# Performance work log

Hardware: AMD Instinct MI355X
Metric: run time of the kernel (lower is better)

## Reference

```python
import jax, jax.numpy as jnp
import numpy as np

B, S, V = 2048, 200, 50257
E, H, EMB = 60, 30, 20  # encode_size, hidden_size, embed_size


def setup_inputs() -> dict:
    key = jax.random.key(0)
    ks = jax.random.split(key, 24)
    emb = jax.random.normal(ks[7], (V, EMB), jnp.float32) * 0.02
    emb = emb.at[3].set(0.0)  # padding_idx=3
    inp = {
        'coverage': jax.random.uniform(ks[0], (B, S), jnp.float32),
        'enc_out': jax.random.normal(ks[1], (B, S, E), jnp.float32),
        'h0': jax.random.normal(ks[2], (1, B, H), jnp.float32),
        'c0': jax.random.normal(ks[3], (1, B, H), jnp.float32),
        'attn': jax.random.uniform(ks[4], (B, S), jnp.float32),
        'dec_input': jax.random.randint(ks[5], (B, 1), 0, V, jnp.int32),
        'enc_inputs': jax.random.randint(ks[6], (B, S), 0, V, jnp.int32),
        'embedding': emb,
        # LSTM (torch gate order i,f,g,o)
        'w_ih': jax.random.normal(ks[8], (4 * H, EMB + E), jnp.float32) * 0.1,
        'w_hh': jax.random.normal(ks[9], (4 * H, H), jnp.float32) * 0.1,
        'b_ih': jax.random.normal(ks[10], (4 * H,), jnp.float32) * 0.1,
        'b_hh': jax.random.normal(ks[11], (4 * H,), jnp.float32) * 0.1,
        # Attention submodule
        'attn_wh_w': jax.random.normal(ks[12], (H, E), jnp.float32) * 0.1,
        'attn_wh_b': jax.random.normal(ks[13], (H,), jnp.float32) * 0.1,
        'attn_ws_w': jax.random.normal(ks[14], (H, H), jnp.float32) * 0.1,
        'attn_ws_b': jax.random.normal(ks[15], (H,), jnp.float32) * 0.1,
        'attn_wc': jax.random.uniform(ks[16], (H,), jnp.float32),
        'attn_v': jax.random.uniform(ks[17], (H,), jnp.float32),
        # pointer-gen params
        'wh': jax.random.uniform(ks[18], (E,), jnp.float32),
        'ws': jax.random.uniform(ks[19], (H,), jnp.float32),
        'wx': jax.random.uniform(ks[20], (EMB,), jnp.float32),
        'v_w': jax.random.normal(ks[21], (V, H), jnp.float32) * 0.02,
        'v_b': jax.random.normal(ks[22], (V,), jnp.float32) * 0.02,
    }
    return inp


def reference(coverage, enc_out, h0, c0, attn, dec_input, enc_inputs, embedding,
              w_ih, w_hh, b_ih, b_hh, attn_wh_w, attn_wh_b, attn_ws_w, attn_ws_b,
              attn_wc, attn_v, wh, ws, wx, v_w, v_b):
    # context = bmm(attn[B,1,S], enc_out[B,S,E]) -> [B,E]
    context = jnp.einsum('bs,bse->be', attn, enc_out)
    embed = embedding[dec_input[:, 0]]              # [B,EMB]
    x = jnp.concatenate([context, embed], axis=-1)  # [B,E+EMB]
    # single-step LSTM (torch gate order i,f,g,o)
    gates = x @ w_ih.T + b_ih + h0[0] @ w_hh.T + b_hh
    i, f, g, o = jnp.split(gates, 4, axis=-1)
    c = jax.nn.sigmoid(f) * c0[0] + jax.nn.sigmoid(i) * jnp.tanh(g)
    h = jax.nn.sigmoid(o) * jnp.tanh(c)             # rnn_out [B,H]
    p_vocab = jax.nn.softmax(h @ v_w.T + v_b, axis=1)   # [B,V]
    p_gen = jax.nn.sigmoid(context @ wh + h @ ws + embed @ wx)[:, None]  # [B,1]
    # attention
    wh_app = enc_out @ attn_wh_w.T + attn_wh_b      # [B,S,H]
    ws_app = (h @ attn_ws_w.T + attn_ws_b)[:, None, :]  # [B,1,H]
    wc_app = coverage[..., None] * attn_wc          # [B,S,H]
    energy = jnp.tanh(wh_app + ws_app + wc_app) @ attn_v  # [B,S]
    new_attn = jax.nn.softmax(energy, axis=1)
    coverage_loss = jnp.sum(jnp.minimum(new_attn, coverage))
    new_coverage = coverage + new_attn
    # scatter copy-attention into vocab space (duplicate idx: arbitrary winner, as torch scatter_)
    rows = jnp.arange(enc_inputs.shape[0])[:, None]
    attn_scores = jnp.zeros((enc_inputs.shape[0], v_w.shape[0]), p_vocab.dtype).at[rows, enc_inputs].set(new_attn)
    output = p_gen * p_vocab + (1.0 - p_gen) * attn_scores
    return output, new_coverage, (h[None], c[None]), new_attn, coverage_loss
```

## Files before the change

### kernel.cpp

```cpp
#include <hip/hip_runtime.h>

#define BB 2048
#define SS 200
#define VV 50257
#define EE 60
#define HH 30
#define EMBD 20
#define XD 80
#define G4 120
#define NCHUNK 100
#define VPAD 51200

#define O_COV ((size_t)BB*VV)
#define O_H   (O_COV + (size_t)BB*SS)
#define O_C   (O_H + (size_t)BB*HH)
#define O_NA  (O_C + (size_t)BB*HH)
#define O_LOSS (O_NA + (size_t)BB*SS)

typedef __attribute__((ext_vector_type(8))) short short8v;
typedef __attribute__((ext_vector_type(4))) float f32x4;
typedef __attribute__((ext_vector_type(4), aligned(4))) float f32x4u;

__device__ __forceinline__ float sigf(float x){ return 1.f/(1.f+__expf(-x)); }

__device__ __forceinline__ short f2bf(float f){
  union { __bf16 h; short s; } u; u.h = (__bf16)f; return u.s;
}

__device__ __forceinline__ float bsum(float v, float* red, int tid){
  #pragma unroll
  for (int off=32; off; off>>=1) v += __shfl_xor(v, off);
  __syncthreads();
  if ((tid&63)==0) red[tid>>6]=v;
  __syncthreads();
  return red[0]+red[1]+red[2]+red[3];
}
__device__ __forceinline__ float bmax(float v, float* red, int tid){
  #pragma unroll
  for (int off=32; off; off>>=1) v = fmaxf(v, __shfl_xor(v, off));
  __syncthreads();
  if ((tid&63)==0) red[tid>>6]=v;
  __syncthreads();
  return fmaxf(fmaxf(red[0],red[1]),fmaxf(red[2],red[3]));
}

__global__ __launch_bounds__(256) void k_pack(
  const float* __restrict__ v_w, const float* __restrict__ v_b,
  short* __restrict__ vw_bf, float* __restrict__ vb_pad)
{
  const int idx = blockIdx.x*256 + threadIdx.x;
  const int col = idx>>2, q = idx&3;
  union { short8v v; short s[8]; } u;
  #pragma unroll
  for (int j=0;j<8;j++){
    int k = q*8+j;
    u.s[j] = (col<VV && k<HH) ? f2bf(v_w[(size_t)col*HH+k]) : (short)0;
  }
  ((short8v*)vw_bf)[idx] = u.v;
  if (q==0) vb_pad[col] = (col<VV) ? v_b[col] : -1e30f;
}

__global__ __launch_bounds__(256) void k_row(
  const float* __restrict__ coverage, const float* __restrict__ enc_out,
  const float* __restrict__ h0, const float* __restrict__ c0,
  const float* __restrict__ attn, const int* __restrict__ dec_input,
  const float* __restrict__ embedding,
  const float* __restrict__ w_ih, const float* __restrict__ w_hh,
  const float* __restrict__ b_ih, const float* __restrict__ b_hh,
  const float* __restrict__ attn_wh_w, const float* __restrict__ attn_wh_b,
  const float* __restrict__ attn_ws_w, const float* __restrict__ attn_ws_b,
  const float* __restrict__ attn_wc, const float* __restrict__ attn_v,
  const float* __restrict__ whv, const float* __restrict__ wsv, const float* __restrict__ wxv,
  float* __restrict__ out, float* __restrict__ pgen_ws,
  float* __restrict__ losspart_ws, short* __restrict__ h_bf)
{
  const int b = blockIdx.x, tid = threadIdx.x;
  __shared__ float enc[SS*61];
  __shared__ float wT[EE*32];
  __shared__ float attn_s[SS], cov_s[SS];
  __shared__ float xls[XD], hls[HH], wsapp[HH], wc_s[HH], v_s[HH], gls[G4];
  __shared__ float ctxp[EE*4];
  __shared__ float red[4];

  {
    const float4* ep = (const float4*)(enc_out + (size_t)b*(SS*EE));
    #pragma unroll
    for (int it=0; it<12; ++it){
      int i = tid + it*256;
      if (i < (SS*EE/4)) {
        float4 v = ep[i];
        int s = i/15, e4 = (i - s*15)*4;
        float* d = &enc[s*61+e4];
        d[0]=v.x; d[1]=v.y; d[2]=v.z; d[3]=v.w;
      }
    }
  }
  if (tid < SS) { attn_s[tid]=attn[(size_t)b*SS+tid]; cov_s[tid]=coverage[(size_t)b*SS+tid]; }
  for (int i=tid; i<EE*HH; i+=256){ int h=i/EE, e=i-h*EE; wT[e*32+h]=attn_wh_w[i]; }
  if (tid >= 256-HH) { int h = tid-(256-HH); wc_s[h]=attn_wc[h]; v_s[h]=attn_v[h]; }
  __syncthreads();

  if (tid < 240){
    int g = tid/60, e = tid - g*60;
    float acc=0.f;
    for (int s=g; s<SS; s+=4) acc += attn_s[s]*enc[s*61+e];
    ctxp[e*4+g]=acc;
  }
  __syncthreads();
  if (tid < EE) xls[tid]=ctxp[tid*4]+ctxp[tid*4+1]+ctxp[tid*4+2]+ctxp[tid*4+3];
  else if (tid < EE+EMBD){
    int k = tid-EE;
    int dix = dec_input[b];
    xls[tid] = embedding[(size_t)dix*EMBD+k];
  }
  __syncthreads();

  if (tid < G4){
    float acc = b_ih[tid]+b_hh[tid];
    const float* wi = w_ih + tid*XD;
    #pragma unroll
    for (int k=0;k<XD;k++) acc += xls[k]*wi[k];
    const float* whh = w_hh + tid*HH;
    const float* h0b = h0 + (size_t)b*HH;
    #pragma unroll
    for (int k=0;k<HH;k++) acc += h0b[k]*whh[k];
    gls[tid]=acc;
  }
  __syncthreads();
  if (tid < HH){
    float c = sigf(gls[tid+HH])*c0[(size_t)b*HH+tid] + sigf(gls[tid])*tanhf(gls[tid+2*HH]);
    float h = sigf(gls[tid+3*HH])*tanhf(c);
    out[O_C+(size_t)b*HH+tid]=c;
    out[O_H+(size_t)b*HH+tid]=h;
    hls[tid]=h;
  }
  __syncthreads();
  if (tid < 4){
    union { short8v v; short s[8]; } u;
    #pragma unroll
    for (int j=0;j<8;j++){ int k=tid*8+j; u.s[j] = (k<HH)? f2bf(hls[k]) : (short)0; }
    ((short8v*)(h_bf + (size_t)b*32))[tid] = u.v;
  }
  if (tid < HH){
    float acc = attn_ws_b[tid] + attn_wh_b[tid];
    const float* w = attn_ws_w + tid*HH;
    #pragma unroll
    for (int k=0;k<HH;k++) acc += hls[k]*w[k];
    wsapp[tid]=acc;
  }
  float pv=0.f;
  if (tid<EE) pv = xls[tid]*whv[tid];
  else if (tid<EE+HH) pv = hls[tid-EE]*wsv[tid-EE];
  else if (tid<EE+HH+EMBD) pv = xls[EE+(tid-EE-HH)]*wxv[tid-EE-HH];
  float pg = sigf(bsum(pv,red,tid));
  if (tid==0) pgen_ws[b]=pg;
  __syncthreads();

  float en = -1e30f;
  if (tid < SS){
    float acc[HH];
    float cv = cov_s[tid];
    #pragma unroll
    for (int h=0;h<HH;h++) acc[h] = wsapp[h] + cv*wc_s[h];
    for (int e=0;e<EE;e++){
      float evv = enc[tid*61+e];
      #pragma unroll
      for (int h=0;h<HH;h++) acc[h] += evv*wT[e*32+h];
    }
    float e2=0.f;
    #pragma unroll
    for (int h=0;h<HH;h++) e2 += tanhf(acc[h])*v_s[h];
    en = e2;
  }
  float mx = bmax(en, red, tid);
  float ex = (tid<SS)? __expf(en-mx) : 0.f;
  float sm = bsum(ex, red, tid);
  float inv = 1.f/sm;
  float lossv = 0.f;
  if (tid<SS){
    float na = ex*inv;
    float cv = cov_s[tid];
    out[O_NA+(size_t)b*SS+tid]=na;
    out[O_COV+(size_t)b*SS+tid]=cv+na;
    lossv = fminf(na,cv);
  }
  float ls = bsum(lossv,red,tid);
  if (tid==0) losspart_ws[b]=ls;
}

__global__ __launch_bounds__(256) void k_vsum(
  const short* __restrict__ vw_bf, const float* __restrict__ vb_pad,
  const short* __restrict__ h_bf, float* __restrict__ partial)
{
  const int tid = threadIdx.x;
  const int w = tid>>6, l = tid&63;
  const int lc = l&15, lg = l>>4;
  const int task = blockIdx.x*4 + w;
  const int rg = task & 127, cg = task >> 7;
  const int rbase = rg*16, cbase = cg*512;

  short8v Bh = *(const short8v*)(h_bf + (size_t)(rbase+lc)*32 + lg*8);

  float ps = 0.f;
  #pragma unroll 4
  for (int t=0;t<32;t++){
    const int ct = cbase + t*16;
    short8v Av = *(const short8v*)(vw_bf + (size_t)(ct+lc)*32 + lg*8);
    f32x4 vb4 = *(const f32x4*)(vb_pad + ct + lg*4);
    f32x4 z = {0.f,0.f,0.f,0.f};
    f32x4 d = __builtin_amdgcn_mfma_f32_16x16x32_bf16(Av, Bh, z, 0,0,0);
    ps += __expf(d[0]+vb4[0]) + __expf(d[1]+vb4[1])
        + __expf(d[2]+vb4[2]) + __expf(d[3]+vb4[3]);
  }
  ps += __shfl_xor(ps,16);
  ps += __shfl_xor(ps,32);
  if (l < 16) partial[(size_t)cg*BB + rbase + lc] = ps;
}

__global__ __launch_bounds__(256) void k_off(
  const float* __restrict__ partial, const float* __restrict__ pgen,
  const float* __restrict__ lp, float* __restrict__ offs,
  float* __restrict__ lossdst)
{
  const int tid = threadIdx.x;
  if (blockIdx.x < 8){
    const int row = blockIdx.x*256 + tid;
    float s=0.f;
    #pragma unroll 5
    for (int c=0;c<NCHUNK;c++) s += partial[(size_t)c*BB + row];
    offs[row] = __logf(pgen[row]) - __logf(s);
  } else {
    __shared__ float red[4];
    float s=0.f;
    for (int i=tid;i<BB;i+=256) s+=lp[i];
    #pragma unroll
    for (int off=32; off; off>>=1) s+=__shfl_xor(s,off);
    if ((tid&63)==0) red[tid>>6]=s;
    __syncthreads();
    if (tid==0) lossdst[0]=red[0]+red[1]+red[2]+red[3];
  }
}

__global__ __launch_bounds__(256) void k_vwrite(
  const short* __restrict__ vw_bf, const float* __restrict__ vb_pad,
  const short* __restrict__ h_bf, const float* __restrict__ offs,
  float* __restrict__ out)
{
  const int tid = threadIdx.x;
  const int w = tid>>6, l = tid&63;
  const int lc = l&15, lg = l>>4;
  const int task = blockIdx.x*4 + w;
  const int rg = task & 127, cg = task >> 7;
  const int rbase = rg*16, cbase = cg*400;

  short8v Bh = *(const short8v*)(h_bf + (size_t)(rbase+lc)*32 + lg*8);
  const int row = rbase + lc;
  const float off = offs[row];
  float* orow = out + (size_t)row*VV;

  #pragma unroll 2
  for (int t=0;t<25;t++){
    const int ct = cbase + t*16;
    const int v0 = ct + lg*4;
    short8v Av = *(const short8v*)(vw_bf + (size_t)(ct+lc)*32 + lg*8);
    f32x4 vb4 = *(const f32x4*)(vb_pad + v0);
    f32x4 z = {0.f,0.f,0.f,0.f};
    f32x4 d = __builtin_amdgcn_mfma_f32_16x16x32_bf16(Av, Bh, z, 0,0,0);
    f32x4 o;
    o[0] = __expf(d[0]+vb4[0]+off);
    o[1] = __expf(d[1]+vb4[1]+off);
    o[2] = __expf(d[2]+vb4[2]+off);
    o[3] = __expf(d[3]+vb4[3]+off);
    if (v0 + 4 <= VV){
      *(f32x4u*)(orow + v0) = o;
    } else {
      #pragma unroll
      for (int r=0;r<4;r++) if (v0 + r < VV) orow[v0+r] = o[r];
    }
  }
}

__global__ __launch_bounds__(256) void k_scatter(
  const int* __restrict__ enc_inputs, const float* __restrict__ pgen,
  const float* __restrict__ na, float* __restrict__ out)
{
  __shared__ int idx_s[SS];
  const int b=blockIdx.x, tid=threadIdx.x;
  if (tid<SS) idx_s[tid]=enc_inputs[(size_t)b*SS+tid];
  __syncthreads();
  if (tid<SS){
    int idx=idx_s[tid];
    bool last=true;
    for (int s2=tid+1;s2<SS;s2++) if (idx_s[s2]==idx){ last=false; break; }
    if (last){
      float add=(1.f-pgen[b])*na[(size_t)b*SS+tid];
      out[(size_t)b*VV+idx]+=add;
    }
  }
}

extern "C" void kernel_launch(void* const* d_in, const int* in_sizes, int n_in,
                              void* d_out, int out_size, void* d_ws, size_t ws_size,
                              hipStream_t stream)
{
  const float* coverage =(const float*)d_in[0];
  const float* enc_out  =(const float*)d_in[1];
  const float* h0       =(const float*)d_in[2];
  const float* c0       =(const float*)d_in[3];
  const float* attn     =(const float*)d_in[4];
  const int*   dec_input=(const int*)d_in[5];
  const int*   enc_inputs=(const int*)d_in[6];
  const float* embedding=(const float*)d_in[7];
  const float* w_ih     =(const float*)d_in[8];
  const float* w_hh     =(const float*)d_in[9];
  const float* b_ih     =(const float*)d_in[10];
  const float* b_hh     =(const float*)d_in[11];
  const float* attn_wh_w=(const float*)d_in[12];
  const float* attn_wh_b=(const float*)d_in[13];
  const float* attn_ws_w=(const float*)d_in[14];
  const float* attn_ws_b=(const float*)d_in[15];
  const float* attn_wc  =(const float*)d_in[16];
  const float* attn_v   =(const float*)d_in[17];
  const float* whv      =(const float*)d_in[18];
  const float* wsv      =(const float*)d_in[19];
  const float* wxv      =(const float*)d_in[20];
  const float* v_w      =(const float*)d_in[21];
  const float* v_b      =(const float*)d_in[22];
  float* out=(float*)d_out;
  float* wsf=(float*)d_ws;
  float* pgen    = wsf;
  float* losspart= wsf + 2048;
  float* offs    = wsf + 4096;
  float* partial = wsf + 6144;
  float* vb_pad  = wsf + 6144 + (size_t)NCHUNK*BB;
  short* vw_bf   = (short*)(vb_pad + VPAD);
  short* h_bf    = vw_bf + (size_t)VPAD*32;

  k_pack<<<VPAD*4/256,256,0,stream>>>(v_w,v_b,vw_bf,vb_pad);

  k_row<<<BB,256,0,stream>>>(coverage,enc_out,h0,c0,attn,dec_input,embedding,
    w_ih,w_hh,b_ih,b_hh,attn_wh_w,attn_wh_b,attn_ws_w,attn_ws_b,attn_wc,attn_v,
    whv,wsv,wxv,out,pgen,losspart,h_bf);

  k_vsum  <<<3200,256,0,stream>>>(vw_bf,vb_pad,h_bf,partial);
  k_off   <<<9,256,0,stream>>>(partial,pgen,losspart,offs,out+O_LOSS);
  k_vwrite<<<4096,256,0,stream>>>(vw_bf,vb_pad,h_bf,offs,out);
  k_scatter<<<BB,256,0,stream>>>(enc_inputs,pgen,out+O_NA,out);
}
```

Before: 357.5 us.

## Align vocab output stores via lane shuffles and coarsen vsum/vwrite work per wave

Output rows of length 50257 are not 16-byte aligned, so the old write kernel used unaligned vector stores. The write kernel now assigns rows sharing the same alignment phase to one wave, writes a small unaligned prologue, and uses cross-lane shuffles to rotate the computed values so each store is an aligned 16-byte write. It also doubles the columns each wave handles in both the sum and write kernels, halving grid sizes, and pads the packed weight buffer for the extra tile read. The cost is extra shuffle and select work per tile, plus fewer waves in flight.

```diff
diff --git a/kernel.cpp b/kernel.cpp
--- a/kernel.cpp
+++ b/kernel.cpp
@@ -8,8 +8,9 @@
 #define EMBD 20
 #define XD 80
 #define G4 120
-#define NCHUNK 100
+#define NCHUNK 50
 #define VPAD 51200
+#define VPAD2 51264
 
 #define O_COV ((size_t)BB*VV)
 #define O_H   (O_COV + (size_t)BB*SS)
@@ -19,7 +20,6 @@
 
 typedef __attribute__((ext_vector_type(8))) short short8v;
 typedef __attribute__((ext_vector_type(4))) float f32x4;
-typedef __attribute__((ext_vector_type(4), aligned(4))) float f32x4u;
 
 __device__ __forceinline__ float sigf(float x){ return 1.f/(1.f+__expf(-x)); }
 
@@ -197,13 +197,13 @@
   const int lc = l&15, lg = l>>4;
   const int task = blockIdx.x*4 + w;
   const int rg = task & 127, cg = task >> 7;
-  const int rbase = rg*16, cbase = cg*512;
+  const int rbase = rg*16, cbase = cg*1024;
 
   short8v Bh = *(const short8v*)(h_bf + (size_t)(rbase+lc)*32 + lg*8);
 
   float ps = 0.f;
   #pragma unroll 4
-  for (int t=0;t<32;t++){
+  for (int t=0;t<64;t++){
     const int ct = cbase + t*16;
     short8v Av = *(const short8v*)(vw_bf + (size_t)(ct+lc)*32 + lg*8);
     f32x4 vb4 = *(const f32x4*)(vb_pad + ct + lg*4);
@@ -251,33 +251,69 @@
   const int lc = l&15, lg = l>>4;
   const int task = blockIdx.x*4 + w;
   const int rg = task & 127, cg = task >> 7;
-  const int rbase = rg*16, cbase = cg*400;
-
-  short8v Bh = *(const short8v*)(h_bf + (size_t)(rbase+lc)*32 + lg*8);
-  const int row = rbase + lc;
+  const int row = (rg>>3)*128 + (rg&7) + 8*lc;
+  const int cbase = cg*800;
+  const int p = (8 - (rg&7)) & 7;
+
+  short8v Bh = *(const short8v*)(h_bf + (size_t)row*32 + lg*8);
   const float off = offs[row];
   float* orow = out + (size_t)row*VV;
 
-  #pragma unroll 2
-  for (int t=0;t<25;t++){
-    const int ct = cbase + t*16;
-    const int v0 = ct + lg*4;
-    short8v Av = *(const short8v*)(vw_bf + (size_t)(ct+lc)*32 + lg*8);
-    f32x4 vb4 = *(const f32x4*)(vb_pad + v0);
-    f32x4 z = {0.f,0.f,0.f,0.f};
-    f32x4 d = __builtin_amdgcn_mfma_f32_16x16x32_bf16(Av, Bh, z, 0,0,0);
+  #define COMPUTE_O(dst, t) {                                            \
+    const int ct_ = cbase + (t)*16;                                      \
+    const int v0_ = ct_ + lg*4;                                          \
+    short8v Av_ = *(const short8v*)(vw_bf + (size_t)(ct_+lc)*32 + lg*8); \
+    f32x4 vb4_ = *(const f32x4*)(vb_pad + v0_);                          \
+    f32x4 z_ = {0.f,0.f,0.f,0.f};                                        \
+    f32x4 d_ = __builtin_amdgcn_mfma_f32_16x16x32_bf16(Av_, Bh, z_, 0,0,0); \
+    dst[0]=__expf(d_[0]+vb4_[0]+off); dst[1]=__expf(d_[1]+vb4_[1]+off);  \
+    dst[2]=__expf(d_[2]+vb4_[2]+off); dst[3]=__expf(d_[3]+vb4_[3]+off); }
+
+  f32x4 cur; COMPUTE_O(cur, 0);
+
+  if (cg==0 && p){
+    #pragma unroll
+    for (int j=0;j<4;j++){
+      const int col = 4*lg + j;
+      if (col < p) orow[col] = cur[j];
+    }
+  }
+
+  const int s1 = (l+16)&63, s2 = (l+32)&63;
+  for (int t=0;t<50;t++){
+    f32x4 nx; COMPUTE_O(nx, t+1);
     f32x4 o;
-    o[0] = __expf(d[0]+vb4[0]+off);
-    o[1] = __expf(d[1]+vb4[1]+off);
-    o[2] = __expf(d[2]+vb4[2]+off);
-    o[3] = __expf(d[3]+vb4[3]+off);
-    if (v0 + 4 <= VV){
-      *(f32x4u*)(orow + v0) = o;
+    if (p == 0){
+      o = cur;
+    } else {
+      f32x4 A, B;
+      #pragma unroll
+      for (int j=0;j<4;j++){
+        float a1 = __shfl(cur[j], s1), b1 = __shfl(nx[j], s1);
+        A[j] = (lg<3)? a1 : b1;
+        float a2 = __shfl(cur[j], s2), b2 = __shfl(nx[j], s2);
+        B[j] = (lg<2)? a2 : b2;
+      }
+      switch(p){
+        case 1: o[0]=cur[1]; o[1]=cur[2]; o[2]=cur[3]; o[3]=A[0]; break;
+        case 2: o[0]=cur[2]; o[1]=cur[3]; o[2]=A[0];   o[3]=A[1]; break;
+        case 3: o[0]=cur[3]; o[1]=A[0];   o[2]=A[1];   o[3]=A[2]; break;
+        case 4: o=A; break;
+        case 5: o[0]=A[1];   o[1]=A[2];   o[2]=A[3];   o[3]=B[0]; break;
+        case 6: o[0]=A[2];   o[1]=A[3];   o[2]=B[0];   o[3]=B[1]; break;
+        default:o[0]=A[3];   o[1]=B[0];   o[2]=B[1];   o[3]=B[2]; break;
+      }
+    }
+    const int g0 = cbase + t*16 + 4*lg + p;
+    if (g0 + 4 <= VV){
+      *(f32x4*)(orow + g0) = o;
     } else {
       #pragma unroll
-      for (int r=0;r<4;r++) if (v0 + r < VV) orow[v0+r] = o[r];
-    }
-  }
+      for (int j=0;j<4;j++) if (g0 + j < VV) orow[g0+j] = o[j];
+    }
+    cur = nx;
+  }
+  #undef COMPUTE_O
 }
 
 __global__ __launch_bounds__(256) void k_scatter(
@@ -333,17 +369,17 @@
   float* offs    = wsf + 4096;
   float* partial = wsf + 6144;
   float* vb_pad  = wsf + 6144 + (size_t)NCHUNK*BB;
-  short* vw_bf   = (short*)(vb_pad + VPAD);
-  short* h_bf    = vw_bf + (size_t)VPAD*32;
-
-  k_pack<<<VPAD*4/256,256,0,stream>>>(v_w,v_b,vw_bf,vb_pad);
+  short* vw_bf   = (short*)(vb_pad + VPAD2);
+  short* h_bf    = vw_bf + (size_t)VPAD2*32;
+
+  k_pack<<<VPAD2*4/256,256,0,stream>>>(v_w,v_b,vw_bf,vb_pad);
 
   k_row<<<BB,256,0,stream>>>(coverage,enc_out,h0,c0,attn,dec_input,embedding,
     w_ih,w_hh,b_ih,b_hh,attn_wh_w,attn_wh_b,attn_ws_w,attn_ws_b,attn_wc,attn_v,
     whv,wsv,wxv,out,pgen,losspart,h_bf);
 
-  k_vsum  <<<3200,256,0,stream>>>(vw_bf,vb_pad,h_bf,partial);
+  k_vsum  <<<1600,256,0,stream>>>(vw_bf,vb_pad,h_bf,partial);
   k_off   <<<9,256,0,stream>>>(partial,pgen,losspart,offs,out+O_LOSS);
-  k_vwrite<<<4096,256,0,stream>>>(vw_bf,vb_pad,h_bf,offs,out);
+  k_vwrite<<<2048,256,0,stream>>>(vw_bf,vb_pad,h_bf,offs,out);
   k_scatter<<<BB,256,0,stream>>>(enc_inputs,pgen,out+O_NA,out);
 }
```

Result: no change. 362.1 us (+1.3%).
